# Performance work log

Hardware: AMD Instinct MI355X
Metric: run time of the kernel (lower is better)

Reference implementation:

```python
import jax, jax.numpy as jnp
import numpy as np

N = 100000
E = 3200000
IN_C, HID_C, OUT_C = 128, 16, 1


def setup_inputs() -> dict:
    key = jax.random.key(0)
    k1, k2, k3, k4, k5, k6 = jax.random.split(key, 6)
    x = jax.random.normal(k1, (N, IN_C), dtype=jnp.float32)
    edge_index = jax.random.randint(k2, (2, E), 0, N, dtype=jnp.int64)
    # Glorot-style init like PyG GCNConv
    W1 = jax.random.normal(k3, (IN_C, HID_C), dtype=jnp.float32) / np.sqrt(IN_C)
    b1 = jnp.zeros((HID_C,), dtype=jnp.float32)
    W2 = jax.random.normal(k4, (HID_C, OUT_C), dtype=jnp.float32) / np.sqrt(HID_C)
    b2 = jnp.zeros((OUT_C,), dtype=jnp.float32)
    return {"x": x, "edge_index": edge_index, "W1": W1, "b1": b1, "W2": W2, "b2": b2}


def _gcn_conv(x, W, b, src, dst, norm):
    # Linear transform first (PyG default flow: transform then aggregate)
    h = x @ W                                  # [N, C_out]
    msg = h[src] * norm[:, None]               # gather + edge-wise scale, [E+N, C_out]
    out = jax.ops.segment_sum(msg, dst, num_segments=N)  # scatter-add, [N, C_out]
    return out + b


def reference(x, edge_index, W1, b1, W2, b2):
    # GCNConv: add self-loops, symmetric normalization D^-1/2 A D^-1/2
    loop = jnp.arange(N, dtype=edge_index.dtype)
    src = jnp.concatenate([edge_index[0], loop])   # [E+N]
    dst = jnp.concatenate([edge_index[1], loop])   # [E+N]
    deg = jax.ops.segment_sum(jnp.ones_like(dst, dtype=x.dtype), dst, num_segments=N)
    dinv = jnp.where(deg > 0, jax.lax.rsqrt(deg), 0.0)
    norm = dinv[src] * dinv[dst]                   # [E+N]

    h = _gcn_conv(x, W1, b1, src, dst, norm)
    h = jax.nn.relu(h)
    # dropout is identity in eval mode (training=False)
    h = _gcn_conv(h, W2, b2, src, dst, norm)
    return jax.nn.sigmoid(h).squeeze()             # [N]
```

## Files before the change

kernel.cpp:

```cpp
#include <hip/hip_runtime.h>
#include <hip/hip_bf16.h>
#include <math.h>

typedef unsigned int u32;

constexpr int N_NODES = 100000;
constexpr int N_EDGES = 3200000;
constexpr int IN_C    = 128;
constexpr int HID_C   = 16;

constexpr int BKT_SHIFT = 11;
constexpr int BKT_NODES = 1 << BKT_SHIFT;
constexpr int NB  = (N_NODES + BKT_NODES - 1) / BKT_NODES;
constexpr int CAP = 67000;
constexpr int EPB = (N_EDGES + 255) / 256;
constexpr int MAXE = (EPB + 1023) / 1024;
constexpr int K_SEG = 8;

__global__ void k_zero(u32* __restrict__ cursor) {
    int i = threadIdx.x;
    if (i < NB) cursor[i] = 0u;
}

__global__ __launch_bounds__(1024) void k_bucket(const int* __restrict__ src,
                                                 const int* __restrict__ dst,
                                                 u32* __restrict__ cursor,
                                                 u32* __restrict__ barr) {
    __shared__ u32 cnt[NB];
    __shared__ u32 base[NB];
    const int e0 = blockIdx.x * EPB;
    const int e1 = min(N_EDGES, e0 + EPB);
    u32 myD[MAXE], myS[MAXE];
#pragma unroll
    for (int i = 0; i < MAXE; ++i) {
        int e = e0 + threadIdx.x + i * 1024;
        if (e < e1) { myD[i] = (u32)dst[e]; myS[i] = (u32)src[e]; }
        else myD[i] = 0xFFFFFFFFu;
    }
    for (int i = threadIdx.x; i < NB; i += blockDim.x) cnt[i] = 0u;
    __syncthreads();
#pragma unroll
    for (int i = 0; i < MAXE; ++i)
        if (myD[i] != 0xFFFFFFFFu) atomicAdd(&cnt[myD[i] >> BKT_SHIFT], 1u);
    __syncthreads();
    for (int i = threadIdx.x; i < NB; i += blockDim.x)
        base[i] = atomicAdd(&cursor[i], cnt[i]);
    __syncthreads();
#pragma unroll
    for (int i = 0; i < MAXE; ++i) {
        if (myD[i] == 0xFFFFFFFFu) continue;
        u32 b = myD[i] >> BKT_SHIFT;
        u32 pos = atomicAdd(&base[b], 1u);
        if (pos < (u32)CAP)
            barr[(size_t)b * CAP + pos] = ((myD[i] & (BKT_NODES - 1)) << 17) | myS[i];
    }
}

__global__ __launch_bounds__(1024) void k_hist(const u32* __restrict__ barr,
                                               const u32* __restrict__ cursor,
                                               u32* __restrict__ seghist) {
    __shared__ u32 h[BKT_NODES];
    const int b = blockIdx.x / K_SEG, s = blockIdx.x % K_SEG;
    const u32 sz = min(cursor[b], (u32)CAP);
    for (int i = threadIdx.x; i < BKT_NODES; i += blockDim.x) h[i] = 0u;
    __syncthreads();
    const u32 e0 = sz * (u32)s / K_SEG, e1 = sz * (u32)(s + 1) / K_SEG;
    const u32* p = barr + (size_t)b * CAP;
    for (u32 e = e0 + threadIdx.x; e < e1; e += blockDim.x)
        atomicAdd(&h[p[e] >> 17], 1u);
    __syncthreads();
    u32* o = seghist + (size_t)(b * K_SEG + s) * BKT_NODES;
    for (int i = threadIdx.x; i < BKT_NODES; i += blockDim.x) o[i] = h[i];
}

__global__ __launch_bounds__(1024) void k_scan(u32* __restrict__ seghist,
                                               const u32* __restrict__ cursor,
                                               int* __restrict__ rowptr,
                                               float* __restrict__ dinv) {
    __shared__ u32 sa[BKT_NODES], sb[BKT_NODES];
    __shared__ u32 s_bb;
    const int b = blockIdx.x;
    const int nbase = b << BKT_SHIFT;
    if (threadIdx.x == 0) {
        u32 t = 0;
        for (int q = 0; q < b; ++q) t += min(cursor[q], (u32)CAP);
        s_bb = t;
        if (b == NB - 1) rowptr[N_NODES] = (int)(t + min(cursor[b], (u32)CAP));
    }
    for (int n = threadIdx.x; n < BKT_NODES; n += blockDim.x) {
        u32 t = 0;
#pragma unroll
        for (int s = 0; s < K_SEG; ++s) {
            size_t idx = (size_t)(b * K_SEG + s) * BKT_NODES + n;
            u32 v = seghist[idx];
            seghist[idx] = t;
            t += v;
        }
        sa[n] = t;
        if (nbase + n < N_NODES) dinv[nbase + n] = rsqrtf(1.0f + (float)t);
    }
    __syncthreads();
    u32 *pa = sa, *pb = sb;
    for (int off = 1; off < BKT_NODES; off <<= 1) {
        for (int n = threadIdx.x; n < BKT_NODES; n += blockDim.x)
            pb[n] = pa[n] + (n >= off ? pa[n - off] : 0u);
        __syncthreads();
        u32* t = pa; pa = pb; pb = t;
    }
    const u32 bb = s_bb;
    for (int n = threadIdx.x; n < BKT_NODES; n += blockDim.x) {
        u32 excl = bb + (n ? pa[n - 1] : 0u);
        if (nbase + n < N_NODES) rowptr[nbase + n] = (int)excl;
#pragma unroll
        for (int s = 0; s < K_SEG; ++s)
            seghist[(size_t)(b * K_SEG + s) * BKT_NODES + n] += excl;
    }
}

__global__ __launch_bounds__(1024) void k_scatter(const u32* __restrict__ barr,
                                                  const u32* __restrict__ cursor,
                                                  const u32* __restrict__ seghist,
                                                  int* __restrict__ adj) {
    __shared__ u32 cur[BKT_NODES];
    const int b = blockIdx.x / K_SEG, s = blockIdx.x % K_SEG;
    const u32 sz = min(cursor[b], (u32)CAP);
    const u32* sbase = seghist + (size_t)(b * K_SEG + s) * BKT_NODES;
    for (int i = threadIdx.x; i < BKT_NODES; i += blockDim.x) cur[i] = sbase[i];
    __syncthreads();
    const u32 e0 = sz * (u32)s / K_SEG, e1 = sz * (u32)(s + 1) / K_SEG;
    const u32* p = barr + (size_t)b * CAP;
    for (u32 e = e0 + threadIdx.x; e < e1; e += blockDim.x) {
        u32 ent = p[e];
        u32 pos = atomicAdd(&cur[ent >> 17], 1u);
        adj[pos] = (int)(ent & 0x1FFFFu);
    }
}

constexpr int NPB = 16;
constexpr int XPAD = 132;
__global__ __launch_bounds__(256) void k_gemm1(const float* __restrict__ x,
                                               const float* __restrict__ W1,
                                               const float* __restrict__ dinv,
                                               __hip_bfloat16* __restrict__ g1b) {
    __shared__ float sx[NPB * XPAD];
    __shared__ float swT[HID_C * XPAD];
    const int nbase = blockIdx.x * NPB;
    {
        const float4* xs = (const float4*)(x + (size_t)nbase * IN_C);
#pragma unroll
        for (int k = 0; k < 2; ++k) {
            int idx = threadIdx.x + k * 256;
            int row = idx >> 5, col4 = idx & 31;
            float4 v = xs[idx];
            ((float4*)(sx + row * XPAD))[col4] = v;
        }
    }
    for (int t = threadIdx.x; t < IN_C * HID_C; t += 256) {
        int j = t >> 4, c = t & 15;
        swT[c * XPAD + j] = W1[t];
    }
    __syncthreads();

    const int n = threadIdx.x >> 4;
    const int c = threadIdx.x & 15;
    const float4* row = (const float4*)(sx + n * XPAD);
    const float4* wc  = (const float4*)(swT + c * XPAD);
    float acc = 0.f;
#pragma unroll
    for (int j = 0; j < IN_C / 4; ++j) {
        float4 v = row[j];
        float4 w = wc[j];
        acc = fmaf(v.x, w.x, acc);
        acc = fmaf(v.y, w.y, acc);
        acc = fmaf(v.z, w.z, acc);
        acc = fmaf(v.w, w.w, acc);
    }
    const int node = nbase + n;
    g1b[node * HID_C + c] = __float2bfloat16(acc * dinv[node]);
}

__global__ void k_agg1(const int* __restrict__ rowptr, const int* __restrict__ adj,
                       const u32* __restrict__ g1u,
                       const float* __restrict__ dinv, const float* __restrict__ b1,
                       const float* __restrict__ W2, float* __restrict__ g2) {
    int t = blockIdx.x * blockDim.x + threadIdx.x;
    int g = t >> 3, l = t & 7;
    if (g >= N_NODES) return;
    int base = rowptr[g], end = rowptr[g + 1];
    u32 sv = g1u[g * 8 + l];
    float a0 = __uint_as_float(sv << 16);
    float a1 = __uint_as_float(sv & 0xFFFF0000u);
    int k = base;
    for (; k + 4 <= end; k += 4) {
        int s0 = adj[k], s1 = adj[k + 1], s2 = adj[k + 2], s3 = adj[k + 3];
        u32 v0 = g1u[s0 * 8 + l], v1 = g1u[s1 * 8 + l];
        u32 v2 = g1u[s2 * 8 + l], v3 = g1u[s3 * 8 + l];
        a0 += __uint_as_float(v0 << 16);
        a1 += __uint_as_float(v0 & 0xFFFF0000u);
        a0 += __uint_as_float(v1 << 16);
        a1 += __uint_as_float(v1 & 0xFFFF0000u);
        a0 += __uint_as_float(v2 << 16);
        a1 += __uint_as_float(v2 & 0xFFFF0000u);
        a0 += __uint_as_float(v3 << 16);
        a1 += __uint_as_float(v3 & 0xFFFF0000u);
    }
    for (; k < end; ++k) {
        u32 v = g1u[adj[k] * 8 + l];
        a0 += __uint_as_float(v << 16);
        a1 += __uint_as_float(v & 0xFFFF0000u);
    }
    float di = dinv[g];
    float2 bb = ((const float2*)b1)[l];
    float2 w  = ((const float2*)W2)[l];
    float h0 = fmaxf(fmaf(a0, di, bb.x), 0.f);
    float h1 = fmaxf(fmaf(a1, di, bb.y), 0.f);
    float part = h0 * w.x + h1 * w.y;
    part += __shfl_xor(part, 1);
    part += __shfl_xor(part, 2);
    part += __shfl_xor(part, 4);
    if (l == 0) g2[g] = part * di;
}

__global__ void k_agg2(const int* __restrict__ rowptr, const int* __restrict__ adj,
                       const float* __restrict__ g2, const float* __restrict__ dinv,
                       const float* __restrict__ b2, float* __restrict__ out) {
    int t = blockIdx.x * blockDim.x + threadIdx.x;
    int g = t >> 2, l = t & 3;
    if (g >= N_NODES) return;
    int base = rowptr[g], end = rowptr[g + 1];
    float acc = (l == 0) ? g2[g] : 0.f;
    for (int k = base + l; k < end; k += 4) acc += g2[adj[k]];
    acc += __shfl_xor(acc, 1);
    acc += __shfl_xor(acc, 2);
    if (l == 0) {
        float v = fmaf(acc, dinv[g], b2[0]);
        out[g] = 1.0f / (1.0f + __expf(-v));
    }
}

extern "C" void kernel_launch(void* const* d_in, const int* in_sizes, int n_in,
                              void* d_out, int out_size, void* d_ws, size_t ws_size,
                              hipStream_t stream) {
    const float* x    = (const float*)d_in[0];
    const int*   edge = (const int*)d_in[1];
    const float* W1   = (const float*)d_in[2];
    const float* b1   = (const float*)d_in[3];
    const float* W2   = (const float*)d_in[4];
    const float* b2   = (const float*)d_in[5];
    float*       out  = (float*)d_out;

    const int* src = edge;
    const int* dst = edge + N_EDGES;

    char* w = (char*)d_ws;
    auto alloc = [&](size_t bytes) { char* r = w; w += (bytes + 255) & ~(size_t)255; return r; };
    u32*   barr       = (u32*)  alloc((size_t)NB * CAP * 4);
    u32*   seghist    = (u32*)  alloc((size_t)NB * K_SEG * BKT_NODES * 4);
    u32*   cursor     = (u32*)  alloc(NB * 4);
    int*   rowptr     = (int*)  alloc((size_t)(N_NODES + 1) * 4);
    float* dinv       = (float*)alloc((size_t)N_NODES * 4);
    int*   adj        = (int*)  alloc((size_t)N_EDGES * 4);
    float*          g2  = (float*)barr;
    __hip_bfloat16* g1b = (__hip_bfloat16*)seghist;
    const u32*      g1u = (const u32*)seghist;

    const int gGemm = N_NODES / NPB;
    const int gAgg1 = (N_NODES * 8 + 255) / 256;
    const int gAgg2 = (N_NODES * 4 + 255) / 256;

    hipLaunchKernelGGL(k_zero,    dim3(1),          dim3(64),   0, stream, cursor);
    hipLaunchKernelGGL(k_bucket,  dim3(256),        dim3(1024), 0, stream, src, dst, cursor, barr);
    hipLaunchKernelGGL(k_hist,    dim3(NB * K_SEG), dim3(1024), 0, stream, barr, cursor, seghist);
    hipLaunchKernelGGL(k_scan,    dim3(NB),         dim3(1024), 0, stream, seghist, cursor, rowptr, dinv);
    hipLaunchKernelGGL(k_scatter, dim3(NB * K_SEG), dim3(1024), 0, stream, barr, cursor, seghist, adj);
    hipLaunchKernelGGL(k_gemm1,   dim3(gGemm),      dim3(256),  0, stream, x, W1, dinv, g1b);
    hipLaunchKernelGGL(k_agg1,    dim3(gAgg1),      dim3(256),  0, stream, rowptr, adj, g1u, dinv, b1, W2, g2);
    hipLaunchKernelGGL(k_agg2,    dim3(gAgg2),      dim3(256),  0, stream, rowptr, adj, g2, dinv, b2, out);
}
```

Measured before the change: 224.9 us.

## Stage bucketed edges in LDS for coalesced writes; widen agg1 gathers to uint2

The bucketing kernel now sorts each block's edges by bucket in shared memory, using per-wave-quarter counters, and then writes them to the global bucket arrays in contiguous runs instead of scattered per-thread stores. A binary search over bucket starts maps each staged entry to its global offset. Separately, the layer-1 aggregation uses 4 lanes per node, each loading 8 bytes (four bf16 features), which halves the thread count and shuffle steps. The LDS staging costs a serial prefix scan on one thread and around 50KB of shared memory, which may reduce occupancy. EPB now assumes the edge count divides evenly by 256.

```diff
diff --git a/kernel.cpp b/kernel.cpp
--- a/kernel.cpp
+++ b/kernel.cpp
@@ -13,9 +13,10 @@
 constexpr int BKT_NODES = 1 << BKT_SHIFT;
 constexpr int NB  = (N_NODES + BKT_NODES - 1) / BKT_NODES;
 constexpr int CAP = 67000;
-constexpr int EPB = (N_EDGES + 255) / 256;
+constexpr int EPB = N_EDGES / 256;
 constexpr int MAXE = (EPB + 1023) / 1024;
 constexpr int K_SEG = 8;
+constexpr int QW = 4;
 
 __global__ void k_zero(u32* __restrict__ cursor) {
     int i = threadIdx.x;
@@ -26,33 +27,54 @@
                                                  const int* __restrict__ dst,
                                                  u32* __restrict__ cursor,
                                                  u32* __restrict__ barr) {
-    __shared__ u32 cnt[NB];
-    __shared__ u32 base[NB];
+    __shared__ u32 cnt4[QW][NB];
+    __shared__ u32 lpre4[QW][NB];
+    __shared__ u32 cur4[QW][NB];
+    __shared__ u32 gbase[NB];
+    __shared__ u32 bstart[NB + 1];
+    __shared__ u32 ents[EPB];
     const int e0 = blockIdx.x * EPB;
-    const int e1 = min(N_EDGES, e0 + EPB);
+    const int q = threadIdx.x >> 8;
     u32 myD[MAXE], myS[MAXE];
 #pragma unroll
     for (int i = 0; i < MAXE; ++i) {
-        int e = e0 + threadIdx.x + i * 1024;
-        if (e < e1) { myD[i] = (u32)dst[e]; myS[i] = (u32)src[e]; }
+        int r = threadIdx.x + i * 1024;
+        if (r < EPB) { myD[i] = (u32)dst[e0 + r]; myS[i] = (u32)src[e0 + r]; }
         else myD[i] = 0xFFFFFFFFu;
     }
-    for (int i = threadIdx.x; i < NB; i += blockDim.x) cnt[i] = 0u;
+    for (int i = threadIdx.x; i < QW * NB; i += 1024) ((u32*)cnt4)[i] = 0u;
     __syncthreads();
 #pragma unroll
     for (int i = 0; i < MAXE; ++i)
-        if (myD[i] != 0xFFFFFFFFu) atomicAdd(&cnt[myD[i] >> BKT_SHIFT], 1u);
-    __syncthreads();
-    for (int i = threadIdx.x; i < NB; i += blockDim.x)
-        base[i] = atomicAdd(&cursor[i], cnt[i]);
+        if (myD[i] != 0xFFFFFFFFu) atomicAdd(&cnt4[q][myD[i] >> BKT_SHIFT], 1u);
+    __syncthreads();
+    if (threadIdx.x == 0) {
+        u32 t = 0;
+        for (int b = 0; b < NB; ++b) {
+            bstart[b] = t;
+            for (int qq = 0; qq < QW; ++qq) { lpre4[qq][b] = t; t += cnt4[qq][b]; }
+        }
+        bstart[NB] = t;
+    }
+    __syncthreads();
+    if (threadIdx.x < NB)
+        gbase[threadIdx.x] = atomicAdd(&cursor[threadIdx.x],
+                                       bstart[threadIdx.x + 1] - bstart[threadIdx.x]);
+    for (int i = threadIdx.x; i < QW * NB; i += 1024) ((u32*)cur4)[i] = ((u32*)lpre4)[i];
     __syncthreads();
 #pragma unroll
     for (int i = 0; i < MAXE; ++i) {
         if (myD[i] == 0xFFFFFFFFu) continue;
         u32 b = myD[i] >> BKT_SHIFT;
-        u32 pos = atomicAdd(&base[b], 1u);
-        if (pos < (u32)CAP)
-            barr[(size_t)b * CAP + pos] = ((myD[i] & (BKT_NODES - 1)) << 17) | myS[i];
+        u32 pos = atomicAdd(&cur4[q][b], 1u);
+        ents[pos] = ((myD[i] & (BKT_NODES - 1)) << 17) | myS[i];
+    }
+    __syncthreads();
+    for (int i = threadIdx.x; i < EPB; i += 1024) {
+        int lo = 0, hi = NB - 1;
+        while (lo < hi) { int mid = (lo + hi + 1) >> 1; if (bstart[mid] <= (u32)i) lo = mid; else hi = mid - 1; }
+        u32 off = gbase[lo] + ((u32)i - bstart[lo]);
+        if (off < (u32)CAP) barr[(size_t)lo * CAP + off] = ents[i];
     }
 }
 
@@ -180,44 +202,57 @@
 }
 
 __global__ void k_agg1(const int* __restrict__ rowptr, const int* __restrict__ adj,
-                       const u32* __restrict__ g1u,
+                       const uint2* __restrict__ g1p,
                        const float* __restrict__ dinv, const float* __restrict__ b1,
                        const float* __restrict__ W2, float* __restrict__ g2) {
     int t = blockIdx.x * blockDim.x + threadIdx.x;
-    int g = t >> 3, l = t & 7;
+    int g = t >> 2, l = t & 3;
     if (g >= N_NODES) return;
     int base = rowptr[g], end = rowptr[g + 1];
-    u32 sv = g1u[g * 8 + l];
-    float a0 = __uint_as_float(sv << 16);
-    float a1 = __uint_as_float(sv & 0xFFFF0000u);
+    uint2 sv = g1p[g * 4 + l];
+    float a0 = __uint_as_float(sv.x << 16);
+    float a1 = __uint_as_float(sv.x & 0xFFFF0000u);
+    float a2 = __uint_as_float(sv.y << 16);
+    float a3 = __uint_as_float(sv.y & 0xFFFF0000u);
     int k = base;
     for (; k + 4 <= end; k += 4) {
         int s0 = adj[k], s1 = adj[k + 1], s2 = adj[k + 2], s3 = adj[k + 3];
-        u32 v0 = g1u[s0 * 8 + l], v1 = g1u[s1 * 8 + l];
-        u32 v2 = g1u[s2 * 8 + l], v3 = g1u[s3 * 8 + l];
-        a0 += __uint_as_float(v0 << 16);
-        a1 += __uint_as_float(v0 & 0xFFFF0000u);
-        a0 += __uint_as_float(v1 << 16);
-        a1 += __uint_as_float(v1 & 0xFFFF0000u);
-        a0 += __uint_as_float(v2 << 16);
-        a1 += __uint_as_float(v2 & 0xFFFF0000u);
-        a0 += __uint_as_float(v3 << 16);
-        a1 += __uint_as_float(v3 & 0xFFFF0000u);
+        uint2 v0 = g1p[s0 * 4 + l], v1 = g1p[s1 * 4 + l];
+        uint2 v2 = g1p[s2 * 4 + l], v3 = g1p[s3 * 4 + l];
+        a0 += __uint_as_float(v0.x << 16);
+        a1 += __uint_as_float(v0.x & 0xFFFF0000u);
+        a2 += __uint_as_float(v0.y << 16);
+        a3 += __uint_as_float(v0.y & 0xFFFF0000u);
+        a0 += __uint_as_float(v1.x << 16);
+        a1 += __uint_as_float(v1.x & 0xFFFF0000u);
+        a2 += __uint_as_float(v1.y << 16);
+        a3 += __uint_as_float(v1.y & 0xFFFF0000u);
+        a0 += __uint_as_float(v2.x << 16);
+        a1 += __uint_as_float(v2.x & 0xFFFF0000u);
+        a2 += __uint_as_float(v2.y << 16);
+        a3 += __uint_as_float(v2.y & 0xFFFF0000u);
+        a0 += __uint_as_float(v3.x << 16);
+        a1 += __uint_as_float(v3.x & 0xFFFF0000u);
+        a2 += __uint_as_float(v3.y << 16);
+        a3 += __uint_as_float(v3.y & 0xFFFF0000u);
     }
     for (; k < end; ++k) {
-        u32 v = g1u[adj[k] * 8 + l];
-        a0 += __uint_as_float(v << 16);
-        a1 += __uint_as_float(v & 0xFFFF0000u);
+        uint2 v = g1p[adj[k] * 4 + l];
+        a0 += __uint_as_float(v.x << 16);
+        a1 += __uint_as_float(v.x & 0xFFFF0000u);
+        a2 += __uint_as_float(v.y << 16);
+        a3 += __uint_as_float(v.y & 0xFFFF0000u);
     }
     float di = dinv[g];
-    float2 bb = ((const float2*)b1)[l];
-    float2 w  = ((const float2*)W2)[l];
-    float h0 = fmaxf(fmaf(a0, di, bb.x), 0.f);
-    float h1 = fmaxf(fmaf(a1, di, bb.y), 0.f);
-    float part = h0 * w.x + h1 * w.y;
+    float2 ba = ((const float2*)b1)[2 * l], bb = ((const float2*)b1)[2 * l + 1];
+    float2 wa = ((const float2*)W2)[2 * l], wb = ((const float2*)W2)[2 * l + 1];
+    float h0 = fmaxf(fmaf(a0, di, ba.x), 0.f);
+    float h1 = fmaxf(fmaf(a1, di, ba.y), 0.f);
+    float h2 = fmaxf(fmaf(a2, di, bb.x), 0.f);
+    float h3 = fmaxf(fmaf(a3, di, bb.y), 0.f);
+    float part = h0 * wa.x + h1 * wa.y + h2 * wb.x + h3 * wb.y;
     part += __shfl_xor(part, 1);
     part += __shfl_xor(part, 2);
-    part += __shfl_xor(part, 4);
     if (l == 0) g2[g] = part * di;
 }
 
@@ -262,10 +297,10 @@
     int*   adj        = (int*)  alloc((size_t)N_EDGES * 4);
     float*          g2  = (float*)barr;
     __hip_bfloat16* g1b = (__hip_bfloat16*)seghist;
-    const u32*      g1u = (const u32*)seghist;
+    const uint2*    g1p = (const uint2*)seghist;
 
     const int gGemm = N_NODES / NPB;
-    const int gAgg1 = (N_NODES * 8 + 255) / 256;
+    const int gAgg1 = (N_NODES * 4 + 255) / 256;
     const int gAgg2 = (N_NODES * 4 + 255) / 256;
 
     hipLaunchKernelGGL(k_zero,    dim3(1),          dim3(64),   0, stream, cursor);
@@ -274,6 +309,6 @@
     hipLaunchKernelGGL(k_scan,    dim3(NB),         dim3(1024), 0, stream, seghist, cursor, rowptr, dinv);
     hipLaunchKernelGGL(k_scatter, dim3(NB * K_SEG), dim3(1024), 0, stream, barr, cursor, seghist, adj);
     hipLaunchKernelGGL(k_gemm1,   dim3(gGemm),      dim3(256),  0, stream, x, W1, dinv, g1b);
-    hipLaunchKernelGGL(k_agg1,    dim3(gAgg1),      dim3(256),  0, stream, rowptr, adj, g1u, dinv, b1, W2, g2);
+    hipLaunchKernelGGL(k_agg1,    dim3(gAgg1),      dim3(256),  0, stream, rowptr, adj, g1p, dinv, b1, W2, g2);
     hipLaunchKernelGGL(k_agg2,    dim3(gAgg2),      dim3(256),  0, stream, rowptr, adj, g2, dinv, b2, out);
 }
```

Result: no change. 228.9 us (+1.8%).
